# Performance work log

Measured on AMD Instinct MI355X. Metric: run time of the kernel, lower is better.

## Reference

```python
import jax, jax.numpy as jnp
import numpy as np

H = 16
DH = 64


def _apply_rotary(x, cos, sin):
    # x: [b, h, s, d]; cos/sin: [s, d//2] -> broadcast to [1, 1, s, d//2]
    x1 = x[..., ::2]
    x2 = x[..., 1::2]
    c = cos[None, None]
    s = sin[None, None]
    rot = jnp.stack([x1 * c - x2 * s, x1 * s + x2 * c], axis=-1)
    return rot.reshape(x.shape)


def setup_inputs() -> dict:
    key = jax.random.key(0)
    ks = jax.random.split(key, 7)
    dim = 1024
    std = 0.02
    x = jax.random.normal(ks[0], (2, 2048, dim), dtype=jnp.float32)
    persistent = jax.random.normal(ks[1], (2, 16, dim), dtype=jnp.float32)
    memory = jax.random.normal(ks[2], (2, 64, dim), dtype=jnp.float32)
    Wq = jax.random.normal(ks[3], (dim, dim), dtype=jnp.float32) * std
    Wk = jax.random.normal(ks[4], (dim, dim), dtype=jnp.float32) * std
    Wv = jax.random.normal(ks[5], (dim, dim), dtype=jnp.float32) * std
    Wo = jax.random.normal(ks[6], (dim, dim), dtype=jnp.float32) * std
    return {"x": x, "persistent": persistent, "memory": memory,
            "Wq": Wq, "Wk": Wk, "Wv": Wv, "Wo": Wo}


def reference(x, persistent, memory, Wq, Wk, Wv, Wo):
    b, L, dim = x.shape
    P = persistent.shape[1] + memory.shape[1]  # prefix_len
    full_x = jnp.concatenate([persistent, memory, x], axis=1)  # [b, P+L, dim]
    S = full_x.shape[1]
    scale = DH ** -0.5

    def proj(W):
        y = full_x @ W.T  # [b, S, dim]
        return y.reshape(b, S, H, DH).transpose(0, 2, 1, 3)  # [b, H, S, DH]

    q = proj(Wq)
    k = proj(Wk)
    v = proj(Wv)

    # RoPE only on the main (input) segment, positions starting at 0.
    pos = jnp.arange(L, dtype=jnp.float32)
    inv_freq = 1.0 / (10000.0 ** (jnp.arange(0, DH, 2, dtype=jnp.float32) / DH))
    freqs = pos[:, None] * inv_freq[None, :]  # [L, DH//2]
    cos, sin = jnp.cos(freqs), jnp.sin(freqs)

    q_main = _apply_rotary(q[:, :, P:], cos, sin)  # [b, H, L, DH]
    k = jnp.concatenate([k[:, :, :P], _apply_rotary(k[:, :, P:], cos, sin)], axis=2)

    # Only main-segment query rows affect the returned output (output[:, P:]).
    # Mask for main queries: prefix keys fully visible; causal within main.
    qi = jnp.arange(L)[:, None]
    kj = jnp.arange(S)[None, :]
    mask = (kj < P) | ((kj - P) <= qi)  # [L, S]

    scores = jnp.einsum('bhqd,bhkd->bhqk', q_main, k) * scale  # [b, H, L, S]
    scores = jnp.where(mask[None, None], scores, -jnp.inf)
    attn = jax.nn.softmax(scores, axis=-1)
    out = jnp.einsum('bhqk,bhkd->bhqd', attn, v)  # [b, H, L, DH]
    out = out.transpose(0, 2, 1, 3).reshape(b, L, dim)
    return out @ Wo.T
```

## Files before the change

### kernel.cpp

```cpp
#include <hip/hip_runtime.h>
#include <math.h>

#define BB    2
#define LL    2048
#define DIM   1024
#define NH    16
#define DHD   64
#define NPER  16
#define NMEM  64
#define PFX   80
#define SS    2128
#define MQKV  (BB*SS)
#define NQKV  3072
#define MOUT  (BB*LL)

typedef __attribute__((ext_vector_type(4)))  float f32x4;
typedef __attribute__((ext_vector_type(16))) float f32x16;
typedef __attribute__((ext_vector_type(8)))  short bf16x8;
typedef unsigned short u16;
typedef unsigned int   u32;

union I4B8 { int4 i; bf16x8 v; };

__device__ __forceinline__ u16 f2bf(float x) {
    union { float f; u32 u; } v; v.f = x;
    return (u16)((v.u + 0x7fffu + ((v.u >> 16) & 1u)) >> 16);
}
__device__ __forceinline__ u32 cvtpk(float lo, float hi) {
    u32 r; asm("v_cvt_pk_bf16_f32 %0, %1, %2" : "=v"(r) : "v"(lo), "v"(hi));
    return r;
}
__device__ __forceinline__ void gload_lds16(const void* g, void* l) {
    __builtin_amdgcn_global_load_lds(
        (__attribute__((address_space(1))) void*)(g),
        (__attribute__((address_space(3))) void*)(l), 16, 0, 0);
}

#define BARRIER()  __builtin_amdgcn_s_barrier()
#define VMCNT8()   asm volatile("s_waitcnt vmcnt(8)")

__global__ __launch_bounds__(256)
void prep_kernel(const float* __restrict__ x,  const float* __restrict__ pe,
                 const float* __restrict__ me, const float* __restrict__ Wq,
                 const float* __restrict__ Wk, const float* __restrict__ Wv,
                 const float* __restrict__ Wo,
                 u16* __restrict__ xbf, u16* __restrict__ wqkv,
                 u16* __restrict__ wobf,
                 float* __restrict__ ropeC, float* __restrict__ ropeS)
{
    const int nthr = gridDim.x * blockDim.x;
    const int t0   = blockIdx.x * blockDim.x + threadIdx.x;

    for (int g = t0; g < MQKV * (DIM / 4); g += nthr) {
        int d4  = g & 255;
        int row = g >> 8;
        int b   = row >= SS;
        int s   = row - b * SS;
        const float* src;
        if (s < NPER)     src = pe + ((size_t)(b * NPER + s)) * DIM;
        else if (s < PFX) src = me + ((size_t)(b * NMEM + (s - NPER))) * DIM;
        else              src = x  + ((size_t)(b * LL   + (s - PFX)))  * DIM;
        float4 v = *reinterpret_cast<const float4*>(src + d4 * 4);
        ushort4 o; o.x = f2bf(v.x); o.y = f2bf(v.y); o.z = f2bf(v.z); o.w = f2bf(v.w);
        *reinterpret_cast<ushort4*>(xbf + (size_t)g * 4) = o;
    }
    for (int g = t0; g < NQKV * (DIM / 4); g += nthr) {
        int row = g >> 8;
        const float* src = (row < 1024) ? (Wq + (size_t)row * DIM)
                         : (row < 2048) ? (Wk + (size_t)(row - 1024) * DIM)
                         :                (Wv + (size_t)(row - 2048) * DIM);
        float4 v = *reinterpret_cast<const float4*>(src + (g & 255) * 4);
        ushort4 o; o.x = f2bf(v.x); o.y = f2bf(v.y); o.z = f2bf(v.z); o.w = f2bf(v.w);
        *reinterpret_cast<ushort4*>(wqkv + (size_t)g * 4) = o;
    }
    for (int g = t0; g < DIM * (DIM / 4); g += nthr) {
        float4 v = *reinterpret_cast<const float4*>(Wo + (size_t)g * 4);
        ushort4 o; o.x = f2bf(v.x); o.y = f2bf(v.y); o.z = f2bf(v.z); o.w = f2bf(v.w);
        *reinterpret_cast<ushort4*>(wobf + (size_t)g * 4) = o;
    }
    for (int i = t0; i < LL * 32; i += nthr) {
        int pos = i >> 5, fi = i & 31;
        float ang = (float)pos * exp2f(-(float)fi * 0.41524101186092029f);
        ropeC[i] = cosf(ang);
        ropeS[i] = sinf(ang);
    }
}

__device__ __forceinline__ void stage_half8(const u16* __restrict__ src, int grow0,
                                            int rmax, int k0, short* ldsbase, int tid)
{
#pragma unroll
    for (int rr = 0; rr < 2; ++rr) {
        int t   = tid + rr * 512;
        int row = t >> 3;
        int c   = t & 7;
        int g = grow0 + row; if (g > rmax) g = rmax;
        gload_lds16(src + (size_t)g * DIM + k0 + ((c ^ (row & 7)) << 3),
                    ldsbase + (tid >> 6) * 512 + rr * 4096);
    }
}

__device__ __forceinline__ bf16x8 ldsfrag(const short* hb, int row, int kbyte)
{
    int byte = (row * 128 + kbyte) ^ ((row & 7) << 4);
    I4B8 t;
    t.i = *reinterpret_cast<const int4*>(reinterpret_cast<const char*>(hb) + byte);
    return t.v;
}

__global__ __launch_bounds__(512, 1)
void qkv_gemm8(const u16* __restrict__ X, const u16* __restrict__ Wq3,
               const float* __restrict__ ropeC, const float* __restrict__ ropeS,
               u16* __restrict__ qb, u16* __restrict__ kb, u16* __restrict__ vb)
{
    __shared__ short Xs[2][16384] __attribute__((aligned(16)));
    __shared__ short Ws[2][16384] __attribute__((aligned(16)));

    const int tid  = threadIdx.x;
    const int lane = tid & 63;
    const int wid  = tid >> 6;
    const int wm   = wid >> 2;
    const int wn   = wid & 3;
    const int bm   = blockIdx.x * 256;
    const int bn   = blockIdx.y * 256;

    f32x4 acc[8][4];
#pragma unroll
    for (int r = 0; r < 8; ++r)
#pragma unroll
        for (int c = 0; c < 4; ++c) acc[r][c] = (f32x4)(0.f);

    stage_half8(X,   bm,       MQKV - 1, 0,  &Xs[0][0],    tid);
    stage_half8(X,   bm + 128, MQKV - 1, 0,  &Xs[0][8192], tid);
    stage_half8(Wq3, bn,       NQKV - 1, 0,  &Ws[0][0],    tid);
    stage_half8(Wq3, bn + 128, NQKV - 1, 0,  &Ws[0][8192], tid);
    stage_half8(X,   bm,       MQKV - 1, 64, &Xs[1][0],    tid);
    stage_half8(X,   bm + 128, MQKV - 1, 64, &Xs[1][8192], tid);
    stage_half8(Wq3, bn,       NQKV - 1, 64, &Ws[1][0],    tid);
    stage_half8(Wq3, bn + 128, NQKV - 1, 64, &Ws[1][8192], tid);
    VMCNT8();
    BARRIER();

    const int frow = lane & 15;
    const int fkb  = (lane >> 4) * 16;
    const int wrow = (wn & 1) * 64;
    const short* XhA[2] = { &Xs[0][0] + wm * 8192,        &Xs[1][0] + wm * 8192 };
    const short* WhA[2] = { &Ws[0][0] + (wn >> 1) * 8192, &Ws[1][0] + (wn >> 1) * 8192 };

    for (int it = 0; it < 8; ++it) {
        int ksA = it * 128 + 128; if (ksA >= 1024) ksA = 0;
        int ksB = it * 128 + 192; if (ksB >= 1024) ksB = 64;
#pragma unroll
        for (int sub = 0; sub < 2; ++sub) {
            const short* Xh = XhA[sub];
            const short* Wh = WhA[sub];
            const int kst = sub ? ksB : ksA;
            short* XsN = &Xs[sub][0];
            short* WsN = &Ws[sub][0];
            bf16x8 xfA[4][2], xfB[4][2], wfA[2][2], wfB[2][2];

#pragma unroll
            for (int r = 0; r < 4; ++r)
#pragma unroll
                for (int ks = 0; ks < 2; ++ks)
                    xfA[r][ks] = ldsfrag(Xh, r * 16 + frow, ks * 64 + fkb);
#pragma unroll
            for (int c = 0; c < 2; ++c)
#pragma unroll
                for (int ks = 0; ks < 2; ++ks)
                    wfA[c][ks] = ldsfrag(Wh, wrow + c * 16 + frow, ks * 64 + fkb);
            BARRIER();
            __builtin_amdgcn_s_setprio(1);
#pragma unroll
            for (int r = 0; r < 4; ++r)
#pragma unroll
                for (int c = 0; c < 2; ++c)
#pragma unroll
                    for (int ks = 0; ks < 2; ++ks)
                        acc[r][c] = __builtin_amdgcn_mfma_f32_16x16x32_bf16(
                            wfA[c][ks], xfA[r][ks], acc[r][c], 0, 0, 0);
            __builtin_amdgcn_s_setprio(0);
            BARRIER();

#pragma unroll
            for (int c = 0; c < 2; ++c)
#pragma unroll
                for (int ks = 0; ks < 2; ++ks)
                    wfB[c][ks] = ldsfrag(Wh, wrow + 32 + c * 16 + frow, ks * 64 + fkb);
            BARRIER();
            __builtin_amdgcn_s_setprio(1);
#pragma unroll
            for (int r = 0; r < 4; ++r)
#pragma unroll
                for (int c = 0; c < 2; ++c)
#pragma unroll
                    for (int ks = 0; ks < 2; ++ks)
                        acc[r][c + 2] = __builtin_amdgcn_mfma_f32_16x16x32_bf16(
                            wfB[c][ks], xfA[r][ks], acc[r][c + 2], 0, 0, 0);
            __builtin_amdgcn_s_setprio(0);
            BARRIER();

#pragma unroll
            for (int r = 0; r < 4; ++r)
#pragma unroll
                for (int ks = 0; ks < 2; ++ks)
                    xfB[r][ks] = ldsfrag(Xh, 64 + r * 16 + frow, ks * 64 + fkb);
            stage_half8(Wq3, bn,       NQKV - 1, kst, WsN,        tid);
            stage_half8(Wq3, bn + 128, NQKV - 1, kst, WsN + 8192, tid);
            BARRIER();
            __builtin_amdgcn_s_setprio(1);
#pragma unroll
            for (int r = 0; r < 4; ++r)
#pragma unroll
                for (int c = 0; c < 2; ++c)
#pragma unroll
                    for (int ks = 0; ks < 2; ++ks)
                        acc[r + 4][c] = __builtin_amdgcn_mfma_f32_16x16x32_bf16(
                            wfA[c][ks], xfB[r][ks], acc[r + 4][c], 0, 0, 0);
            __builtin_amdgcn_s_setprio(0);
            BARRIER();

            stage_half8(X, bm,       MQKV - 1, kst, XsN,        tid);
            stage_half8(X, bm + 128, MQKV - 1, kst, XsN + 8192, tid);
            BARRIER();
            __builtin_amdgcn_s_setprio(1);
#pragma unroll
            for (int r = 0; r < 4; ++r)
#pragma unroll
                for (int c = 0; c < 2; ++c)
#pragma unroll
                    for (int ks = 0; ks < 2; ++ks)
                        acc[r + 4][c + 2] = __builtin_amdgcn_mfma_f32_16x16x32_bf16(
                            wfB[c][ks], xfB[r][ks], acc[r + 4][c + 2], 0, 0, 0);
            __builtin_amdgcn_s_setprio(0);
            VMCNT8();
            BARRIER();
        }
    }

    const int cbase = bn + wn * 64 + ((lane >> 4) << 2);
    const int rbase = bm + wm * 128 + (lane & 15);
    const int which = bn >> 10;

#pragma unroll
    for (int xr = 0; xr < 8; ++xr) {
        const int row = rbase + xr * 16;
        if (row >= MQKV) continue;
        const int b = row >= SS;
        const int s = row - b * SS;
#pragma unroll
        for (int wc = 0; wc < 4; ++wc) {
            const int c0 = cbase + wc * 16;
            float v0 = acc[xr][wc][0], v1 = acc[xr][wc][1];
            float v2 = acc[xr][wc][2], v3 = acc[xr][wc][3];
            const int nn = c0 & 1023;
            const int h  = nn >> 6;
            const int dh = nn & 63;
            if (which != 2 && s >= PFX) {
                const int pos = s - PFX;
                float2 cs = *reinterpret_cast<const float2*>(ropeC + pos * 32 + (dh >> 1));
                float2 sn = *reinterpret_cast<const float2*>(ropeS + pos * 32 + (dh >> 1));
                float t0 = v0 * cs.x - v1 * sn.x;
                v1 = v0 * sn.x + v1 * cs.x; v0 = t0;
                float t2 = v2 * cs.y - v3 * sn.y;
                v3 = v2 * sn.y + v3 * cs.y; v2 = t2;
            }
            ushort4 o;
            o.x = f2bf(v0); o.y = f2bf(v1); o.z = f2bf(v2); o.w = f2bf(v3);
            if (which == 0) {
                if (s >= PFX)
                    *reinterpret_cast<ushort4*>(
                        &qb[(((size_t)b * NH + h) * LL + (s - PFX)) * DHD + dh]) = o;
            } else if (which == 1) {
                *reinterpret_cast<ushort4*>(
                    &kb[(((size_t)b * NH + h) * SS + s) * DHD + dh]) = o;
            } else {
                *reinterpret_cast<ushort4*>(
                    &vb[(((size_t)b * NH + h) * SS + s) * DHD + dh]) = o;
            }
        }
    }
}

__global__ __launch_bounds__(256)
void wo_gemm(const u16* __restrict__ A, const u16* __restrict__ Bw,
             float* __restrict__ outp)
{
    __shared__ short As[128 * 32] __attribute__((aligned(16)));
    __shared__ short Bs[128 * 32] __attribute__((aligned(16)));

    const int tid  = threadIdx.x;
    const int lane = tid & 63;
    const int wid  = tid >> 6;
    const int wr   = wid >> 1, wc = wid & 1;
    const int bm   = blockIdx.x * 128;
    const int bn   = blockIdx.y * 128;

    f32x4 acc[4][4];
#pragma unroll
    for (int m = 0; m < 4; ++m)
#pragma unroll
        for (int n = 0; n < 4; ++n) acc[m][n] = (f32x4)(0.f);

    const int r0 = wid * 32 + (lane >> 2);
    const int cc = (lane & 3) * 8;

    for (int k0 = 0; k0 < DIM; k0 += 32) {
        gload_lds16(A + (size_t)(bm + r0) * DIM + k0 + cc, As + wid * 1024);
        gload_lds16(A + (size_t)(bm + r0 + 16) * DIM + k0 + cc, As + wid * 1024 + 512);
        gload_lds16(Bw + (size_t)(bn + r0) * DIM + k0 + cc, Bs + wid * 1024);
        gload_lds16(Bw + (size_t)(bn + r0 + 16) * DIM + k0 + cc, Bs + wid * 1024 + 512);
        __syncthreads();

        bf16x8 wf[4], xf[4];
#pragma unroll
        for (int m = 0; m < 4; ++m)
            wf[m] = *reinterpret_cast<const bf16x8*>(
                Bs + (wr * 64 + m * 16 + (lane & 15)) * 32 + (lane >> 4) * 8);
#pragma unroll
        for (int n = 0; n < 4; ++n)
            xf[n] = *reinterpret_cast<const bf16x8*>(
                As + (wc * 64 + n * 16 + (lane & 15)) * 32 + (lane >> 4) * 8);
#pragma unroll
        for (int m = 0; m < 4; ++m)
#pragma unroll
            for (int n = 0; n < 4; ++n)
                acc[m][n] = __builtin_amdgcn_mfma_f32_16x16x32_bf16(
                    wf[m], xf[n], acc[m][n], 0, 0, 0);
        __syncthreads();
    }

    const int cbase = bn + wr * 64 + ((lane >> 4) << 2);
    const int rbase = bm + wc * 64 + (lane & 15);
#pragma unroll
    for (int n = 0; n < 4; ++n) {
        const int row = rbase + n * 16;
#pragma unroll
        for (int m = 0; m < 4; ++m) {
            const int c0 = cbase + m * 16;
            *reinterpret_cast<float4*>(&outp[(size_t)row * DIM + c0]) =
                make_float4(acc[m][n][0], acc[m][n][1], acc[m][n][2], acc[m][n][3]);
        }
    }
}

__device__ __forceinline__ void attn_load_tile(
    const u16* __restrict__ kb0, const u16* __restrict__ vb0,
    int j0, int tid, int vp, int vo,
    int4& k0r, int4& k1r, int4& v0r, int4& v1r)
{
    int key0 = tid >> 3,        o0 = tid & 7;
    int c1   = tid + 256;
    int key1 = c1 >> 3,         o1 = c1 & 7;
    int jg0 = j0 + key0; if (jg0 > SS - 1) jg0 = SS - 1;
    int jg1 = j0 + key1; if (jg1 > SS - 1) jg1 = SS - 1;
    k0r = *reinterpret_cast<const int4*>(kb0 + (size_t)jg0 * DHD + o0 * 8);
    k1r = *reinterpret_cast<const int4*>(kb0 + (size_t)jg1 * DHD + o1 * 8);
    int ja  = j0 + 2 * vp;     if (ja  > SS - 1) ja  = SS - 1;
    int jb2 = j0 + 2 * vp + 1; if (jb2 > SS - 1) jb2 = SS - 1;
    v0r = *reinterpret_cast<const int4*>(vb0 + (size_t)ja  * DHD + vo * 8);
    v1r = *reinterpret_cast<const int4*>(vb0 + (size_t)jb2 * DHD + vo * 8);
}

__global__ __launch_bounds__(256, 2)
void attn_mfma(const u16* __restrict__ qb, const u16* __restrict__ kb,
               const u16* __restrict__ vb, u16* __restrict__ ctx)
{
    __shared__ u16 Ks[64 * 64] __attribute__((aligned(16)));
    __shared__ u16 Vt[64 * 64] __attribute__((aligned(16)));
    __shared__ u16 Ot[4][32 * 72] __attribute__((aligned(16)));

    const int tid  = threadIdx.x;
    const int lane = tid & 63;
    const int wv   = tid >> 6;
    const int h    = lane >> 5;
    const int ql   = lane & 31;

    const int bh   = blockIdx.y;
    const int b    = bh >> 4;
    const int head = bh & 15;
    int qt = blockIdx.x;
    if (b) qt = 15 - qt;
    const int q0  = qt * 128;
    const int q0w = q0 + 32 * wv;

    const u16* qrow = qb + ((size_t)bh * LL + q0w + ql) * DHD;
    bf16x8 qf[4];
#pragma unroll
    for (int ks = 0; ks < 4; ++ks) {
        I4B8 t; t.i = *reinterpret_cast<const int4*>(qrow + ks * 16 + h * 8);
        qf[ks] = t.v;
    }

    f32x16 oa0 = (f32x16)(0.f), oa1 = (f32x16)(0.f);
    float m = -INFINITY, l = 0.f;

    const u16* kb0 = kb + (size_t)bh * SS * DHD;
    const u16* vb0 = vb + (size_t)bh * SS * DHD;

    const int ntiles   = (PFX + q0 + 128 + 63) / 64;
    const int wave_lim = PFX + q0w + 31;
    const int vp = tid & 31;
    const int vo = tid >> 5;

    int4 rk0, rk1, rv0, rv1;
    attn_load_tile(kb0, vb0, 0, tid, vp, vo, rk0, rk1, rv0, rv1);

    for (int kt = 0; kt < ntiles; ++kt) {
        const int j0 = kt * 64;

        {
            int key0 = tid >> 3, o0 = tid & 7;
            int c1 = tid + 256;
            int key1 = c1 >> 3, o1 = c1 & 7;
            *reinterpret_cast<int4*>((char*)Ks + ((key0 * 128 + o0 * 16) ^ ((key0 & 7) << 4))) = rk0;
            *reinterpret_cast<int4*>((char*)Ks + ((key1 * 128 + o1 * 16) ^ ((key1 & 7) << 4))) = rk1;
            const u16* pa = reinterpret_cast<const u16*>(&rv0);
            const u16* pb = reinterpret_cast<const u16*>(&rv1);
#pragma unroll
            for (int d = 0; d < 8; ++d) {
                u32 wpk = (u32)pa[d] | ((u32)pb[d] << 16);
                int dh = vo * 8 + d;
                *reinterpret_cast<u32*>((char*)Vt + ((dh * 128 + vp * 4) ^ ((d & 7) << 4))) = wpk;
            }
        }
        __syncthreads();

        int4 nk0, nk1, nv0, nv1;
        attn_load_tile(kb0, vb0, j0 + 64, tid, vp, vo, nk0, nk1, nv0, nv1);

        if (j0 <= wave_lim) {
            f32x16 s0 = (f32x16)(0.f), s1 = (f32x16)(0.f);
            __builtin_amdgcn_s_setprio(1);
#pragma unroll
            for (int ks = 0; ks < 4; ++ks) {
                I4B8 k0, k1;
                k0.i = *reinterpret_cast<const int4*>(
                    (const char*)Ks + (((ql) * 128 + ks * 32 + h * 16) ^ ((ql & 7) << 4)));
                k1.i = *reinterpret_cast<const int4*>(
                    (const char*)Ks + (((32 + ql) * 128 + ks * 32 + h * 16) ^ ((ql & 7) << 4)));
                s0 = __builtin_amdgcn_mfma_f32_32x32x16_bf16(k0.v, qf[ks], s0, 0, 0, 0);
                s1 = __builtin_amdgcn_mfma_f32_32x32x16_bf16(k1.v, qf[ks], s1, 0, 0, 0);
            }
            __builtin_amdgcn_s_setprio(0);
            float sv[32];
#pragma unroll
            for (int i = 0; i < 16; ++i) { sv[i] = s0[i] * 0.125f; sv[16 + i] = s1[i] * 0.125f; }
            if (j0 + 63 > PFX + q0w) {
                const int lim = PFX + q0w + ql - j0;
#pragma unroll
                for (int i = 0; i < 32; ++i) {
                    int koff = ((i >= 16) ? 32 : 0) + (i & 3) + 8 * ((i & 15) >> 2) + 4 * h;
                    if (koff > lim) sv[i] = -INFINITY;
                }
            }
            float mt = sv[0];
#pragma unroll
            for (int i = 1; i < 32; ++i) mt = fmaxf(mt, sv[i]);
            mt = fmaxf(mt, __shfl_xor(mt, 32));
            float mn = fmaxf(m, mt);
            float f = __expf(m - mn);
            m = mn;
            float ls = 0.f;
            u32 W0[8], W1[8];
#pragma unroll
            for (int i = 0; i < 8; ++i) {
                float pa = __expf(sv[2 * i] - m);
                float pb = __expf(sv[2 * i + 1] - m);
                ls += pa + pb;
                W0[i] = cvtpk(pa, pb);
            }
#pragma unroll
            for (int i = 0; i < 8; ++i) {
                float pa = __expf(sv[16 + 2 * i] - m);
                float pb = __expf(sv[16 + 2 * i + 1] - m);
                ls += pa + pb;
                W1[i] = cvtpk(pa, pb);
            }
            ls += __shfl_xor(ls, 32);
            l = l * f + ls;
#pragma unroll
            for (int i = 0; i < 16; ++i) { oa0[i] *= f; oa1[i] *= f; }

            __builtin_amdgcn_s_setprio(1);
#pragma unroll
            for (int ks = 0; ks < 4; ++ks) {
                const int a4 = (ks & 1) * 4;
                u32 A0, A1, A2, A3;
                if (ks < 2) { A0 = W0[a4]; A1 = W0[a4 + 1]; A2 = W0[a4 + 2]; A3 = W0[a4 + 3]; }
                else        { A0 = W1[a4]; A1 = W1[a4 + 1]; A2 = W1[a4 + 2]; A3 = W1[a4 + 3]; }
                asm volatile("v_permlane32_swap_b32 %0, %1" : "+v"(A0), "+v"(A2));
                asm volatile("v_permlane32_swap_b32 %0, %1" : "+v"(A1), "+v"(A3));
                I4B8 pf; pf.i = make_int4((int)A0, (int)A1, (int)A2, (int)A3);
                I4B8 vf0, vf1;
                vf0.i = *reinterpret_cast<const int4*>(
                    (const char*)Vt + (((ql) * 128 + ks * 32 + h * 16) ^ ((ql & 7) << 4)));
                vf1.i = *reinterpret_cast<const int4*>(
                    (const char*)Vt + (((32 + ql) * 128 + ks * 32 + h * 16) ^ ((ql & 7) << 4)));
                oa0 = __builtin_amdgcn_mfma_f32_32x32x16_bf16(vf0.v, pf.v, oa0, 0, 0, 0);
                oa1 = __builtin_amdgcn_mfma_f32_32x32x16_bf16(vf1.v, pf.v, oa1, 0, 0, 0);
            }
            __builtin_amdgcn_s_setprio(0);
        }
        __syncthreads();
        rk0 = nk0; rk1 = nk1; rv0 = nv0; rv1 = nv1;
    }

    const float inv = 1.f / l;
    u16* orow = &Ot[wv][ql * 72];
#pragma unroll
    for (int i = 0; i < 8; ++i) {
        u32 w0 = cvtpk(oa0[2 * i] * inv, oa0[2 * i + 1] * inv);
        u32 w1 = cvtpk(oa1[2 * i] * inv, oa1[2 * i + 1] * inv);
        int dh0 = ((2 * i) & 3) + 8 * ((2 * i) >> 2) + 4 * h;
        *reinterpret_cast<u32*>(&orow[dh0]) = w0;
        *reinterpret_cast<u32*>(&orow[32 + dh0]) = w1;
    }
    const int rr = lane >> 1, hh = lane & 1;
    const u16* src = &Ot[wv][rr * 72 + hh * 32];
    u16* dst = ctx + ((size_t)(b * LL + q0 + 32 * wv + rr)) * DIM + head * DHD + hh * 32;
#pragma unroll
    for (int i = 0; i < 4; ++i) {
        int4 t = *reinterpret_cast<const int4*>(src + i * 8);
        *reinterpret_cast<int4*>(dst + i * 8) = t;
    }
}

extern "C" void kernel_launch(void* const* d_in, const int* in_sizes, int n_in,
                              void* d_out, int out_size, void* d_ws, size_t ws_size,
                              hipStream_t stream)
{
    const float* x  = (const float*)d_in[0];
    const float* pe = (const float*)d_in[1];
    const float* me = (const float*)d_in[2];
    const float* Wq = (const float*)d_in[3];
    const float* Wk = (const float*)d_in[4];
    const float* Wv = (const float*)d_in[5];
    const float* Wo = (const float*)d_in[6];
    float* out = (float*)d_out;

    u16* xbf  = (u16*)d_ws;
    u16* wqkv = xbf + (size_t)MQKV * DIM;
    u16* wobf = wqkv + (size_t)NQKV * DIM;
    float* ropeC = (float*)(wobf + (size_t)DIM * DIM);
    float* ropeS = ropeC + LL * 32;
    u16* qbf = (u16*)(ropeS + LL * 32);
    u16* kbf = qbf + (size_t)BB * NH * LL * DHD;
    u16* vbf = kbf + (size_t)BB * NH * SS * DHD;
    u16* ctx = vbf + (size_t)BB * NH * SS * DHD;

    hipLaunchKernelGGL(prep_kernel, dim3(2048), dim3(256), 0, stream,
                       x, pe, me, Wq, Wk, Wv, Wo, xbf, wqkv, wobf, ropeC, ropeS);
    hipLaunchKernelGGL(qkv_gemm8, dim3((MQKV + 255) / 256, NQKV / 256), dim3(512), 0, stream,
                       xbf, wqkv, ropeC, ropeS, qbf, kbf, vbf);
    hipLaunchKernelGGL(attn_mfma, dim3(16, BB * NH), dim3(256), 0, stream,
                       qbf, kbf, vbf, ctx);
    hipLaunchKernelGGL(wo_gemm, dim3(MOUT / 128, DIM / 128), dim3(256), 0, stream,
                       ctx, wobf, out);
}
```

Baseline: 151.5 us.

## Double-buffer K/V shared tiles in attention to drop one barrier per iteration

Converts the attention kernel's K and V LDS tiles into two ping-pong buffers. Each iteration writes the next tile into the idle buffer and issues the global load two tiles ahead, then computes on the current buffer, leaving one __syncthreads per iteration instead of two. This aims to overlap LDS staging with MFMA compute and cut barrier stalls. In exchange it doubles K/V shared memory, which could reduce occupancy at 2 blocks per CU, and the prefetch clamps indices past the sequence end.

```diff
diff --git a/kernel.cpp b/kernel.cpp
--- a/kernel.cpp
+++ b/kernel.cpp
@@ -366,8 +366,8 @@
 void attn_mfma(const u16* __restrict__ qb, const u16* __restrict__ kb,
                const u16* __restrict__ vb, u16* __restrict__ ctx)
 {
-    __shared__ u16 Ks[64 * 64] __attribute__((aligned(16)));
-    __shared__ u16 Vt[64 * 64] __attribute__((aligned(16)));
+    __shared__ u16 Ks[2][64 * 64] __attribute__((aligned(16)));
+    __shared__ u16 Vt[2][64 * 64] __attribute__((aligned(16)));
     __shared__ u16 Ot[4][32 * 72] __attribute__((aligned(16)));
 
     const int tid  = threadIdx.x;
@@ -402,47 +402,57 @@
     const int wave_lim = PFX + q0w + 31;
     const int vp = tid & 31;
     const int vo = tid >> 5;
+    const int key0 = tid >> 3, o0 = tid & 7;
+    const int key1 = (tid + 256) >> 3, o1 = (tid + 256) & 7;
 
     int4 rk0, rk1, rv0, rv1;
+
+    auto stage_write = [&](int nb, const int4& a, const int4& c,
+                           const int4& va, const int4& vbq) {
+        char* KD = (char*)&Ks[nb][0];
+        *reinterpret_cast<int4*>(KD + ((key0 * 128 + o0 * 16) ^ ((key0 & 7) << 4))) = a;
+        *reinterpret_cast<int4*>(KD + ((key1 * 128 + o1 * 16) ^ ((key1 & 7) << 4))) = c;
+        char* VD = (char*)&Vt[nb][0];
+        const u16* pa = reinterpret_cast<const u16*>(&va);
+        const u16* pb = reinterpret_cast<const u16*>(&vbq);
+#pragma unroll
+        for (int d = 0; d < 8; ++d) {
+            u32 wpk = (u32)pa[d] | ((u32)pb[d] << 16);
+            int dh = vo * 8 + d;
+            *reinterpret_cast<u32*>(VD + ((dh * 128 + vp * 4) ^ ((d & 7) << 4))) = wpk;
+        }
+    };
+
     attn_load_tile(kb0, vb0, 0, tid, vp, vo, rk0, rk1, rv0, rv1);
+    stage_write(0, rk0, rk1, rv0, rv1);
+    attn_load_tile(kb0, vb0, 64, tid, vp, vo, rk0, rk1, rv0, rv1);
+    __syncthreads();
 
     for (int kt = 0; kt < ntiles; ++kt) {
-        const int j0 = kt * 64;
-
-        {
-            int key0 = tid >> 3, o0 = tid & 7;
-            int c1 = tid + 256;
-            int key1 = c1 >> 3, o1 = c1 & 7;
-            *reinterpret_cast<int4*>((char*)Ks + ((key0 * 128 + o0 * 16) ^ ((key0 & 7) << 4))) = rk0;
-            *reinterpret_cast<int4*>((char*)Ks + ((key1 * 128 + o1 * 16) ^ ((key1 & 7) << 4))) = rk1;
-            const u16* pa = reinterpret_cast<const u16*>(&rv0);
-            const u16* pb = reinterpret_cast<const u16*>(&rv1);
-#pragma unroll
-            for (int d = 0; d < 8; ++d) {
-                u32 wpk = (u32)pa[d] | ((u32)pb[d] << 16);
-                int dh = vo * 8 + d;
-                *reinterpret_cast<u32*>((char*)Vt + ((dh * 128 + vp * 4) ^ ((d & 7) << 4))) = wpk;
-            }
-        }
-        __syncthreads();
-
-        int4 nk0, nk1, nv0, nv1;
-        attn_load_tile(kb0, vb0, j0 + 64, tid, vp, vo, nk0, nk1, nv0, nv1);
+        const int j0  = kt * 64;
+        const int cur = kt & 1;
+
+        stage_write(cur ^ 1, rk0, rk1, rv0, rv1);
+        attn_load_tile(kb0, vb0, j0 + 128, tid, vp, vo, rk0, rk1, rv0, rv1);
 
         if (j0 <= wave_lim) {
+            const char* KB = (const char*)&Ks[cur][0];
+            const char* VB = (const char*)&Vt[cur][0];
+
             f32x16 s0 = (f32x16)(0.f), s1 = (f32x16)(0.f);
             __builtin_amdgcn_s_setprio(1);
 #pragma unroll
             for (int ks = 0; ks < 4; ++ks) {
                 I4B8 k0, k1;
                 k0.i = *reinterpret_cast<const int4*>(
-                    (const char*)Ks + (((ql) * 128 + ks * 32 + h * 16) ^ ((ql & 7) << 4)));
+                    KB + (((ql) * 128 + ks * 32 + h * 16) ^ ((ql & 7) << 4)));
                 k1.i = *reinterpret_cast<const int4*>(
-                    (const char*)Ks + (((32 + ql) * 128 + ks * 32 + h * 16) ^ ((ql & 7) << 4)));
+                    KB + (((32 + ql) * 128 + ks * 32 + h * 16) ^ ((ql & 7) << 4)));
                 s0 = __builtin_amdgcn_mfma_f32_32x32x16_bf16(k0.v, qf[ks], s0, 0, 0, 0);
                 s1 = __builtin_amdgcn_mfma_f32_32x32x16_bf16(k1.v, qf[ks], s1, 0, 0, 0);
             }
             __builtin_amdgcn_s_setprio(0);
+
             float sv[32];
 #pragma unroll
             for (int i = 0; i < 16; ++i) { sv[i] = s0[i] * 0.125f; sv[16 + i] = s1[i] * 0.125f; }
@@ -494,16 +504,15 @@
                 I4B8 pf; pf.i = make_int4((int)A0, (int)A1, (int)A2, (int)A3);
                 I4B8 vf0, vf1;
                 vf0.i = *reinterpret_cast<const int4*>(
-                    (const char*)Vt + (((ql) * 128 + ks * 32 + h * 16) ^ ((ql & 7) << 4)));
+                    VB + (((ql) * 128 + ks * 32 + h * 16) ^ ((ql & 7) << 4)));
                 vf1.i = *reinterpret_cast<const int4*>(
-                    (const char*)Vt + (((32 + ql) * 128 + ks * 32 + h * 16) ^ ((ql & 7) << 4)));
+                    VB + (((32 + ql) * 128 + ks * 32 + h * 16) ^ ((ql & 7) << 4)));
                 oa0 = __builtin_amdgcn_mfma_f32_32x32x16_bf16(vf0.v, pf.v, oa0, 0, 0, 0);
                 oa1 = __builtin_amdgcn_mfma_f32_32x32x16_bf16(vf1.v, pf.v, oa1, 0, 0, 0);
             }
             __builtin_amdgcn_s_setprio(0);
         }
         __syncthreads();
-        rk0 = nk0; rk1 = nk1; rv0 = nv0; rv1 = nv1;
     }
 
     const float inv = 1.f / l;
```

New measurement: 152.3 us. No clear change (+0.5%).
